# Kernel tuning notes

Hardware: AMD Instinct MI355X
Metric: run time of the kernel (lower is better)

Reference implementation:

```python
import jax, jax.numpy as jnp
import numpy as np

N_WIRES = 4
# Fixed realization of tq.RandomLayer(n_ops=8, wires=[0..3]):
# a deterministic sequence of 8 parameterized gates with angles theta[k].
RANDOM_OPS = [
    ("rx", (0,)), ("ry", (1,)), ("rz", (3,)), ("crx", (0, 2)),
    ("ry", (3,)), ("rx", (2,)), ("crx", (1, 3)), ("rz", (0,)),
]


def _ry(t):
    c = jnp.cos(t / 2).astype(jnp.complex64)
    s = jnp.sin(t / 2).astype(jnp.complex64)
    return jnp.stack([jnp.stack([c, -s]), jnp.stack([s, c])])


def _rx(t):
    c = jnp.cos(t / 2).astype(jnp.complex64)
    s = jnp.sin(t / 2).astype(jnp.complex64)
    return jnp.stack([jnp.stack([c, -1j * s]), jnp.stack([-1j * s, c])])


def _rz(t):
    e0 = jnp.exp(-1j * (t / 2)).astype(jnp.complex64)
    e1 = jnp.exp(1j * (t / 2)).astype(jnp.complex64)
    z = jnp.zeros((), jnp.complex64)
    return jnp.stack([jnp.stack([e0, z]), jnp.stack([z, e1])])


def _crx(t):
    U = _rx(t)
    z2 = jnp.zeros((2, 2), jnp.complex64)
    i2 = jnp.eye(2, dtype=jnp.complex64)
    return jnp.concatenate([jnp.concatenate([i2, z2], 1), jnp.concatenate([z2, U], 1)], 0)


def _apply_1q(psi, U, w):
    # psi: (N,2,2,2,2); apply 2x2 gate on wire w
    psi = jnp.moveaxis(psi, 1 + w, -1)
    psi = psi @ U.T
    return jnp.moveaxis(psi, -1, 1 + w)


def _apply_2q(psi, U4, w1, w2):
    psi = jnp.moveaxis(psi, (1 + w1, 1 + w2), (-2, -1))
    shp = psi.shape
    psi = (psi.reshape(shp[:-2] + (4,)) @ U4.T).reshape(shp)
    return jnp.moveaxis(psi, (-2, -1), (1 + w1, 1 + w2))


def _quanv_forward(x, theta, W, b):
    B = x.shape[0]
    img = x.reshape(B, 28, 28)
    # 2x2 stride-2 patches, order [x[r,c], x[r,c+1], x[r+1,c], x[r+1,c+1]]
    patches = img.reshape(B, 14, 2, 14, 2).transpose(0, 1, 3, 2, 4).reshape(B * 196, 4)
    # RY-encoded product state: ry(a)|0> = [cos(a/2), sin(a/2)]
    half = patches * 0.5
    c = jnp.cos(half).astype(jnp.complex64)
    s = jnp.sin(half).astype(jnp.complex64)
    v = jnp.stack([c, s], axis=-1)  # (N, 4 wires, 2)
    psi = jnp.einsum('na,nb,nc,nd->nabcd', v[:, 0], v[:, 1], v[:, 2], v[:, 3])
    gate_fns = {"rx": _rx, "ry": _ry, "rz": _rz}
    for k, (name, wires) in enumerate(RANDOM_OPS):
        t = theta[k]
        if name == "crx":
            psi = _apply_2q(psi, _crx(t), wires[0], wires[1])
        else:
            psi = _apply_1q(psi, gate_fns[name](t), wires[0])
    probs = (psi.real ** 2 + psi.imag ** 2).reshape(-1, 16)  # (N,16)
    # PauliZ expectation per wire; wire 0 is the most significant bit
    idx = jnp.arange(16)
    bits = (idx[:, None] >> (3 - jnp.arange(N_WIRES)[None, :])) & 1
    z_table = (1.0 - 2.0 * bits).astype(jnp.float32)  # (16,4)
    meas = probs @ z_table  # (N,4)
    feats = meas.reshape(B, 196 * 4)  # (B,784), patch-major like torch.cat
    logits = feats @ W.T + b
    return jax.nn.log_softmax(logits, axis=-1)


def setup_inputs() -> dict:
    key = jax.random.key(0)
    k1, k2, k3 = jax.random.split(key, 3)
    B = 2048
    x = jax.random.normal(k1, (B, 1, 28, 28), jnp.float32)
    theta = jax.random.normal(k2, (8,), jnp.float32)
    W = jax.random.normal(k3, (10, 784), jnp.float32) * 0.02
    b = jnp.zeros((10,), jnp.float32)
    return {"x": x, "theta": theta, "W": W, "b": b}


def reference(x, theta, W, b):
    return _quanv_forward(x, theta, W, b)
```

## Files before the change

kernel.cpp:

```cpp
#include <hip/hip_runtime.h>
#include <math.h>


__global__ __launch_bounds__(256) void quanv_fused_kernel(
    const float* __restrict__ xin,
    const float* __restrict__ theta,
    const float* __restrict__ Wm,
    const float* __restrict__ bv,
    float* __restrict__ out,
    int B)
{
    __shared__ float kc[9];
    __shared__ __align__(16) float4 feats[4][196];

    const int t  = threadIdx.x;
    const int b0 = blockIdx.x * 4;

    if (t == 0) {
        const float t0 = theta[0], t1 = theta[1], t2 = theta[2], t3 = theta[3];
        const float t4 = theta[4], t5 = theta[5], t6 = theta[6];
        const float c5g = cosf(t5), c35 = cosf(t3 + t5);
        const float c6 = cosf(t6), s6 = sinf(t6);
        kc[0] = cosf(t0);
        kc[1] = t1;
        kc[2] = 0.5f * (c5g + c35);
        kc[3] = 0.5f * cosf(t0) * (c5g - c35);
        kc[4] = 0.5f * (1.f + c6);
        kc[5] = 0.5f * (1.f - c6);
        kc[6] = cosf(t4);
        kc[7] = -sinf(t4) * cosf(t2);
        kc[8] = 0.5f * s6 * sinf(t2);
    }
    __syncthreads();

    if (t < 196) {
        const int pi = t / 14, pj = t % 14;
        const float* base = xin + (size_t)b0 * 784 + pi * 56 + pj * 2;

        float2 rA[4], rB[4];
#pragma unroll
        for (int i = 0; i < 4; ++i) {
            rA[i] = *(const float2*)(base + i * 784);
            rB[i] = *(const float2*)(base + i * 784 + 28);
        }

        const float k0 = kc[0], th1 = kc[1], A = kc[2], Bc = kc[3];
        const float C1 = kc[4], C2 = kc[5], K1 = kc[6], K2 = kc[7], C5 = kc[8];

#pragma unroll
        for (int i = 0; i < 4; ++i) {
            const float ca0 = __cosf(rA[i].x);
            const float u   = __cosf(rA[i].y + th1);
            const float ca2 = __cosf(rB[i].x);
            float sa3, ca3;
            __sincosf(rB[i].y, &sa3, &ca3);

            const float m0 = k0 * ca0;
            const float m2 = ca2 * fmaf(Bc, ca0, A);
            const float zu = fmaf(K1, ca3, K2 * sa3);
            const float m3 = fmaf(fmaf(C2, u, C1), zu, C5 * sa3 * (1.f - u));

            feats[i][t] = make_float4(m0, u, m2, m3);
        }
    }
    __syncthreads();

    const int w = t >> 6, l = t & 63;

    float acc[10];
#pragma unroll
    for (int c = 0; c < 10; ++c) acc[c] = 0.f;

    const float4* fw = feats[w];
    const float4* W4 = (const float4*)Wm;

#pragma unroll
    for (int k = 0; k < 3; ++k) {
        const int p = l + 64 * k;
        const float4 f = fw[p];
#pragma unroll
        for (int c = 0; c < 10; ++c) {
            const float4 wv = W4[c * 196 + p];
            acc[c] = fmaf(f.w, wv.w, fmaf(f.z, wv.z,
                     fmaf(f.y, wv.y, fmaf(f.x, wv.x, acc[c]))));
        }
    }
    if (l < 4) {
        const int p = 192 + l;
        const float4 f = fw[p];
#pragma unroll
        for (int c = 0; c < 10; ++c) {
            const float4 wv = W4[c * 196 + p];
            acc[c] = fmaf(f.w, wv.w, fmaf(f.z, wv.z,
                     fmaf(f.y, wv.y, fmaf(f.x, wv.x, acc[c]))));
        }
    }

    float logit[10];
#pragma unroll
    for (int c = 0; c < 10; ++c) {
        float v = acc[c];
        v += __shfl_xor(v, 32, 64);
        v += __shfl_xor(v, 16, 64);
        v += __shfl_xor(v, 8, 64);
        v += __shfl_xor(v, 4, 64);
        v += __shfl_xor(v, 2, 64);
        v += __shfl_xor(v, 1, 64);
        logit[c] = v + bv[c];
    }

    float mx = -1e30f;
#pragma unroll
    for (int c = 0; c < 10; ++c) mx = fmaxf(mx, logit[c]);
    float sum = 0.f;
#pragma unroll
    for (int c = 0; c < 10; ++c) sum += expf(logit[c] - mx);
    const float ls = logf(sum);

    const int img = b0 + w;
    if (l == 0 && img < B) {
        float* o = out + (size_t)img * 10;
#pragma unroll
        for (int c = 0; c < 10; ++c) o[c] = logit[c] - mx - ls;
    }
}

extern "C" void kernel_launch(void* const* d_in, const int* in_sizes, int n_in,
                              void* d_out, int out_size, void* d_ws, size_t ws_size,
                              hipStream_t stream) {
    const float* x     = (const float*)d_in[0];
    const float* theta = (const float*)d_in[1];
    const float* W     = (const float*)d_in[2];
    const float* bias  = (const float*)d_in[3];
    float* out         = (float*)d_out;

    const int B = in_sizes[0] / 784;
    const int grid = (B + 3) / 4;
    quanv_fused_kernel<<<grid, 256, 0, stream>>>(x, theta, W, bias, out, B);
}
```

Measured before the change: 12.90 us.

## Compute patch features per wavefront in registers, removing shared memory and barriers

Each wavefront now owns one image: every lane loads its own patches, computes the quantum features in registers, and feeds them straight into the dot product with W. This removes the shared-memory feature buffer, both block barriers and the single-thread theta precompute, which every lane now does redundantly. It also switches to fast exp/log intrinsics and spreads the output store across ten lanes. In exchange, all 64 lanes do the feature work instead of 196 of 256 threads, and each thread does extra transcendental math for theta.

```diff
diff --git a/kernel.cpp b/kernel.cpp
--- a/kernel.cpp
+++ b/kernel.cpp
@@ -10,74 +10,66 @@
     float* __restrict__ out,
     int B)
 {
-    __shared__ float kc[9];
-    __shared__ __align__(16) float4 feats[4][196];
+    const int t = threadIdx.x;
+    const int w = t >> 6, l = t & 63;
+    const int img = blockIdx.x * 4 + w;
+    if (img >= B) return;
 
-    const int t  = threadIdx.x;
-    const int b0 = blockIdx.x * 4;
+    const float* ib = xin + (size_t)img * 784;
+    const bool tail = (l < 4);
 
-    if (t == 0) {
-        const float t0 = theta[0], t1 = theta[1], t2 = theta[2], t3 = theta[3];
-        const float t4 = theta[4], t5 = theta[5], t6 = theta[6];
-        const float c5g = cosf(t5), c35 = cosf(t3 + t5);
-        const float c6 = cosf(t6), s6 = sinf(t6);
-        kc[0] = cosf(t0);
-        kc[1] = t1;
-        kc[2] = 0.5f * (c5g + c35);
-        kc[3] = 0.5f * cosf(t0) * (c5g - c35);
-        kc[4] = 0.5f * (1.f + c6);
-        kc[5] = 0.5f * (1.f - c6);
-        kc[6] = cosf(t4);
-        kc[7] = -sinf(t4) * cosf(t2);
-        kc[8] = 0.5f * s6 * sinf(t2);
+    float2 rA[4], rB[4];
+#pragma unroll
+    for (int k = 0; k < 3; ++k) {
+        const int p = l + 64 * k;
+        const int pi = p / 14, pj = p % 14;
+        const float* pr = ib + pi * 56 + pj * 2;
+        rA[k] = *(const float2*)pr;
+        rB[k] = *(const float2*)(pr + 28);
     }
-    __syncthreads();
+    {
+        const int p = tail ? (192 + l) : l;
+        const int pi = p / 14, pj = p % 14;
+        const float* pr = ib + pi * 56 + pj * 2;
+        rA[3] = *(const float2*)pr;
+        rB[3] = *(const float2*)(pr + 28);
+    }
 
-    if (t < 196) {
-        const int pi = t / 14, pj = t % 14;
-        const float* base = xin + (size_t)b0 * 784 + pi * 56 + pj * 2;
+    const float t0 = theta[0], th1 = theta[1], t2 = theta[2], t3 = theta[3];
+    const float t4 = theta[4], t5 = theta[5], t6 = theta[6];
+    const float c5g = cosf(t5), c35 = cosf(t3 + t5);
+    const float c6 = cosf(t6), s6 = sinf(t6);
+    const float k0 = cosf(t0);
+    const float A  = 0.5f * (c5g + c35);
+    const float Bc = 0.5f * k0 * (c5g - c35);
+    const float C1 = 0.5f * (1.f + c6);
+    const float C2 = 0.5f * (1.f - c6);
+    const float K1 = cosf(t4);
+    const float K2 = -sinf(t4) * cosf(t2);
+    const float C5 = 0.5f * s6 * sinf(t2);
 
-        float2 rA[4], rB[4];
-#pragma unroll
-        for (int i = 0; i < 4; ++i) {
-            rA[i] = *(const float2*)(base + i * 784);
-            rB[i] = *(const float2*)(base + i * 784 + 28);
-        }
-
-        const float k0 = kc[0], th1 = kc[1], A = kc[2], Bc = kc[3];
-        const float C1 = kc[4], C2 = kc[5], K1 = kc[6], K2 = kc[7], C5 = kc[8];
-
-#pragma unroll
-        for (int i = 0; i < 4; ++i) {
-            const float ca0 = __cosf(rA[i].x);
-            const float u   = __cosf(rA[i].y + th1);
-            const float ca2 = __cosf(rB[i].x);
-            float sa3, ca3;
-            __sincosf(rB[i].y, &sa3, &ca3);
-
-            const float m0 = k0 * ca0;
-            const float m2 = ca2 * fmaf(Bc, ca0, A);
-            const float zu = fmaf(K1, ca3, K2 * sa3);
-            const float m3 = fmaf(fmaf(C2, u, C1), zu, C5 * sa3 * (1.f - u));
-
-            feats[i][t] = make_float4(m0, u, m2, m3);
-        }
-    }
-    __syncthreads();
-
-    const int w = t >> 6, l = t & 63;
+    auto featf = [&](float2 a, float2 b) -> float4 {
+        const float ca0 = __cosf(a.x);
+        const float u   = __cosf(a.y + th1);
+        const float ca2 = __cosf(b.x);
+        float sa3, ca3;
+        __sincosf(b.y, &sa3, &ca3);
+        const float m0 = k0 * ca0;
+        const float m2 = ca2 * fmaf(Bc, ca0, A);
+        const float zu = fmaf(K1, ca3, K2 * sa3);
+        const float m3 = fmaf(fmaf(C2, u, C1), zu, C5 * sa3 * (1.f - u));
+        return make_float4(m0, u, m2, m3);
+    };
 
     float acc[10];
 #pragma unroll
     for (int c = 0; c < 10; ++c) acc[c] = 0.f;
 
-    const float4* fw = feats[w];
     const float4* W4 = (const float4*)Wm;
-
 #pragma unroll
     for (int k = 0; k < 3; ++k) {
+        const float4 f = featf(rA[k], rB[k]);
         const int p = l + 64 * k;
-        const float4 f = fw[p];
 #pragma unroll
         for (int c = 0; c < 10; ++c) {
             const float4 wv = W4[c * 196 + p];
@@ -85,9 +77,9 @@
                      fmaf(f.y, wv.y, fmaf(f.x, wv.x, acc[c]))));
         }
     }
-    if (l < 4) {
+    if (tail) {
+        const float4 f = featf(rA[3], rB[3]);
         const int p = 192 + l;
-        const float4 f = fw[p];
 #pragma unroll
         for (int c = 0; c < 10; ++c) {
             const float4 wv = W4[c * 196 + p];
@@ -114,14 +106,14 @@
     for (int c = 0; c < 10; ++c) mx = fmaxf(mx, logit[c]);
     float sum = 0.f;
 #pragma unroll
-    for (int c = 0; c < 10; ++c) sum += expf(logit[c] - mx);
-    const float ls = logf(sum);
+    for (int c = 0; c < 10; ++c) sum += __expf(logit[c] - mx);
+    const float ls = __logf(sum);
 
-    const int img = b0 + w;
-    if (l == 0 && img < B) {
-        float* o = out + (size_t)img * 10;
+    if (l < 10) {
+        float v = logit[9];
 #pragma unroll
-        for (int c = 0; c < 10; ++c) o[c] = logit[c] - mx - ls;
+        for (int c = 8; c >= 0; --c) v = (l == c) ? logit[c] : v;
+        out[(size_t)img * 10 + l] = v - mx - ls;
     }
 }
 
```

New measurement: 10.71 us. -17.0%, faster.
